# Kernel tuning notes

Measured on AMD Instinct MI355X. Metric: run time of the kernel, lower is better.

The kernel has to match this reference:

```python
import jax, jax.numpy as jnp
import numpy as np

H = 12  # num_heads


def setup_inputs() -> dict:
    key = jax.random.key(0)
    ks = jax.random.split(key, 5)
    B, N, C = 4, 1025, 768
    x = jax.random.normal(ks[0], (B, N, C), jnp.float32)
    g_info = jax.random.normal(ks[1], (2, 2, C), jnp.float32)
    # parameters (torch Linear equivalents, pre-transposed to x @ W layout)
    w_qkv = jax.random.normal(ks[2], (C, 3 * C), jnp.float32) * (C ** -0.5)
    w_proj = jax.random.normal(ks[3], (C, C), jnp.float32) * (C ** -0.5)
    b_proj = jax.random.normal(ks[4], (C,), jnp.float32) * 0.02
    return {"x": x, "g_info": g_info, "w_qkv": w_qkv, "w_proj": w_proj, "b_proj": b_proj}


def _forward(x, g_info, w_qkv, w_proj, b_proj):
    B, N, C = x.shape
    Dh = C // H
    qkv = (x @ w_qkv).reshape(B, N, 3, H, Dh)
    q, k, v = qkv[:, :, 0], qkv[:, :, 1], qkv[:, :, 2]  # (B,N,H,Dh)

    # grounding query from first g_info layer, row 0
    q_g = g_info[0].reshape(-1, H, Dh)[0]  # (H,Dh)

    # num_reserved = 1 (cls token); "pure" = patch tokens
    q_pure = q[:, 1:]  # (B,M,H,Dh)
    qn = q_pure / jnp.linalg.norm(q_pure, axis=-1, keepdims=True)
    qgn = q_g / jnp.linalg.norm(q_g, axis=-1, keepdims=True)
    q_sim = (qn * qgn).sum(-1).mean(-1)  # (B,M): cosine sim averaged over heads
    q_sim = (q_sim - q_sim.min()) / (q_sim.max() - q_sim.min())  # global min-max norm
    pos = q_sim > 0.9   # (B,M) per-batch routing mask
    neg = ~pos
    # a token index is kept in a group if ANY batch element routes it there
    keep_pos = pos.any(axis=0)  # (M,)
    keep_neg = neg.any(axis=0)

    scale = Dh ** -0.5  # xformers memory_efficient_attention internal scale

    def group_attn(gmask, keep):
        # gmask (B,M) bool; keep (M,) bool. Faithful to the torch gather:
        # kept-but-other-batch tokens participate with ZEROED q/k/v.
        m = gmask[..., None, None].astype(x.dtype)  # (B,M,1,1)
        qg = jnp.concatenate([q[:, :1], q_pure * m], axis=1)      # (B,N,H,Dh)
        kg = jnp.concatenate([k[:, :1], k[:, 1:] * m], axis=1)
        vg = jnp.concatenate([v[:, :1], v[:, 1:] * m], axis=1)
        key_keep = jnp.concatenate([jnp.ones((1,), bool), keep])  # cls always kept
        logits = jnp.einsum('bqhd,bkhd->bhqk', qg, kg) * scale
        logits = jnp.where(key_keep[None, None, None, :], logits, -jnp.inf)
        attn = jax.nn.softmax(logits, axis=-1)
        return jnp.einsum('bhqk,bkhd->bqhd', attn, vg)  # (B,N,H,Dh)

    out_pos = group_attn(pos, keep_pos)
    out_neg = group_attn(neg, keep_neg)

    # indices in neither group stay zero (cannot happen since pos|neg covers all).
    body = jnp.where(keep_neg[None, :, None, None], out_neg[:, 1:],
                     jnp.where(keep_pos[None, :, None, None], out_pos[:, 1:],
                               jnp.zeros_like(out_pos[:, 1:])))
    cls = (out_pos[:, :1] + out_neg[:, :1]) * 0.5
    xo = jnp.concatenate([cls, body], axis=1).reshape(B, N, C)
    return xo @ w_proj + b_proj


def reference(x, g_info, w_qkv, w_proj, b_proj):
    return (_forward(x, g_info, w_qkv, w_proj, b_proj), g_info[1:])
```

## Files before the change

kernel.cpp:

```cpp
#include <hip/hip_runtime.h>
#include <math.h>

typedef unsigned short ushort_t;
typedef short s16x8 __attribute__((ext_vector_type(8)));
typedef float f32x4 __attribute__((ext_vector_type(4)));

#define MFMA16(a, b, c) __builtin_amdgcn_mfma_f32_16x16x32_bf16(a, b, c, 0, 0, 0)

#define BATCH 4
#define SEQ   1025
#define CH    768
#define HEADS 12
#define NBH   48
#define NKPAD 1088
#define NTILE 17
#define NQB   34
#define MROWS 4100
#define SCALE2 0.18033688011112042f

__device__ __forceinline__ ushort_t f2bf(float f) {
    unsigned u = __builtin_bit_cast(unsigned, f);
    u += 0x7FFFu + ((u >> 16) & 1u);
    return (ushort_t)(u >> 16);
}
__device__ __forceinline__ unsigned cvt_pk_bf16(float lo, float hi) {
    unsigned r;
    asm("v_cvt_pk_bf16_f32 %0, %1, %2" : "=v"(r) : "v"(lo), "v"(hi));
    return r;
}
__device__ __forceinline__ float max3f(float a, float b, float c) {
    float r;
    asm("v_max3_f32 %0, %1, %2, %3" : "=v"(r) : "v"(a), "v"(b), "v"(c));
    return r;
}
__device__ __forceinline__ float fast_exp2(float x) {
    float r; asm("v_exp_f32 %0, %1" : "=v"(r) : "v"(x)); return r;
}

__global__ __launch_bounds__(256) void gemm_f32(
    const float* __restrict__ A, const float* __restrict__ Bm,
    float* __restrict__ Cm, int M, int K, int ldb, int Nn)
{
    __shared__ float As[32][68];
    __shared__ float Bs[32][64];
    int t = threadIdx.x;
    int m0 = blockIdx.y * 64, n0 = blockIdx.x * 64;
    int ty = t >> 4, tx = t & 15;
    int laRow = t >> 2, laK = (t & 3) * 4;
    int lbK = t >> 4, lbN = (t & 15) * 4;
    float acc[4][4] = {};
    for (int k0 = 0; k0 < K; k0 += 32) {
        int arow = m0 + laRow;
        #pragma unroll
        for (int half = 0; half < 2; ++half) {
            float4 av = make_float4(0.f, 0.f, 0.f, 0.f);
            if (arow < M) av = *(const float4*)(A + (size_t)arow * K + k0 + laK + 16 * half);
            As[laK + 16 * half + 0][laRow] = av.x;
            As[laK + 16 * half + 1][laRow] = av.y;
            As[laK + 16 * half + 2][laRow] = av.z;
            As[laK + 16 * half + 3][laRow] = av.w;
            *(float4*)&Bs[lbK + 16 * half][lbN] =
                *(const float4*)(Bm + (size_t)(k0 + lbK + 16 * half) * ldb + n0 + lbN);
        }
        __syncthreads();
        #pragma unroll
        for (int kk = 0; kk < 32; ++kk) {
            float4 a4 = *(const float4*)&As[kk][ty * 4];
            float4 b4 = *(const float4*)&Bs[kk][tx * 4];
            float a[4] = {a4.x, a4.y, a4.z, a4.w};
            float b[4] = {b4.x, b4.y, b4.z, b4.w};
            #pragma unroll
            for (int i = 0; i < 4; ++i)
                #pragma unroll
                for (int j = 0; j < 4; ++j) acc[i][j] += a[i] * b[j];
        }
        __syncthreads();
    }
    #pragma unroll
    for (int i = 0; i < 4; ++i) {
        int row = m0 + ty * 4 + i;
        if (row >= M) continue;
        #pragma unroll
        for (int j = 0; j < 4; ++j)
            Cm[(size_t)row * Nn + n0 + tx * 4 + j] = acc[i][j];
    }
}

__global__ __launch_bounds__(256) void convx(const float* __restrict__ x,
                                             ushort_t* __restrict__ xb, int n4)
{
    int i = blockIdx.x * 256 + threadIdx.x;
    if (i >= n4) return;
    float4 v = ((const float4*)x)[i];
    ushort_t o[4] = {f2bf(v.x), f2bf(v.y), f2bf(v.z), f2bf(v.w)};
    *(uint2*)(xb + (size_t)i * 4) = *(const uint2*)o;
}

__global__ __launch_bounds__(256) void convT(const float* __restrict__ src, int ld,
                                             int c0, ushort_t* __restrict__ dst)
{
    __shared__ float tile[32][33];
    int k0 = blockIdx.x * 32, n0 = blockIdx.y * 32;
    int t = threadIdx.x, tx = t & 31, ty = t >> 5;
    #pragma unroll
    for (int i = 0; i < 32; i += 8)
        tile[ty + i][tx] = src[(size_t)(k0 + ty + i) * ld + c0 + n0 + tx];
    __syncthreads();
    #pragma unroll
    for (int i = 0; i < 32; i += 8)
        dst[(size_t)(n0 + ty + i) * CH + k0 + tx] = f2bf(tile[tx][ty + i]);
}

__global__ __launch_bounds__(256) void qconv(const float* __restrict__ qf,
                                             ushort_t* __restrict__ qtb)
{
    int i = blockIdx.x * 256 + threadIdx.x;
    if (i >= MROWS * CH / 8) return;
    int row = i / (CH / 8);
    int rem = i % (CH / 8);
    int b = row / SEQ, tok = row % SEQ;
    int h = rem >> 3, d8 = (rem & 7) * 8;
    const float* src = qf + (size_t)row * CH + h * 64 + d8;
    ushort_t o[8];
    #pragma unroll
    for (int j = 0; j < 8; ++j) o[j] = f2bf(src[j]);
    *(uint4*)(qtb + ((size_t)(b * HEADS + h) * NKPAD + tok) * 64 + d8) =
        *(const uint4*)o;
}

template<int MODE>
__global__ __launch_bounds__(256) void mfma_gemm(
    const ushort_t* __restrict__ A, const ushort_t* __restrict__ B,
    ushort_t* __restrict__ kbuf, ushort_t* __restrict__ vtbuf,
    const float* __restrict__ bias, float* __restrict__ outp)
{
    __shared__ __align__(16) ushort_t As[128][40];
    __shared__ __align__(16) ushort_t Bs[64][40];
    const int NT = (MODE == 0) ? 24 : 12;
    int t = threadIdx.x, w = t >> 6, l = t & 63;
    int l15 = l & 15, lhi = l >> 4;
    int wr = w >> 1, wc = w & 1;

    int lin = blockIdx.x, logical;
    if (MODE == 0) {
        logical = (lin & 7) * 99 + (lin >> 3);
    } else {
        int xcd = lin & 7, idx = lin >> 3;
        logical = (xcd < 4 ? xcd * 50 : 200 + (xcd - 4) * 49) + idx;
    }
    int m0 = (logical / NT) * 128;
    int n0 = (logical % NT) * 64;

    int trow = t >> 2, tcol = (t & 3) * 8;
    f32x4 acc[4][2] = {};

    for (int k0 = 0; k0 < CH; k0 += 32) {
        uint4 a0v = make_uint4(0, 0, 0, 0), a1v = make_uint4(0, 0, 0, 0);
        int ar0 = m0 + trow, ar1 = m0 + trow + 64;
        if (ar0 < MROWS) a0v = *(const uint4*)(A + (size_t)ar0 * CH + k0 + tcol);
        if (ar1 < MROWS) a1v = *(const uint4*)(A + (size_t)ar1 * CH + k0 + tcol);
        uint4 bv = *(const uint4*)(B + (size_t)(n0 + trow) * CH + k0 + tcol);
        if (k0) __syncthreads();
        *(uint4*)&As[trow][tcol] = a0v;
        *(uint4*)&As[trow + 64][tcol] = a1v;
        *(uint4*)&Bs[trow][tcol] = bv;
        __syncthreads();
        s16x8 af[4], bf[2];
        #pragma unroll
        for (int i = 0; i < 4; ++i)
            af[i] = *(const s16x8*)&As[wr * 64 + 16 * i + l15][lhi * 8];
        #pragma unroll
        for (int j = 0; j < 2; ++j)
            bf[j] = *(const s16x8*)&Bs[wc * 32 + 16 * j + l15][lhi * 8];
        #pragma unroll
        for (int i = 0; i < 4; ++i)
            #pragma unroll
            for (int j = 0; j < 2; ++j)
                acc[i][j] = MFMA16(af[i], bf[j], acc[i][j]);
    }

    #pragma unroll
    for (int i = 0; i < 4; ++i)
        #pragma unroll
        for (int j = 0; j < 2; ++j)
            #pragma unroll
            for (int r = 0; r < 4; ++r) {
                int m = m0 + wr * 64 + 16 * i + lhi * 4 + r;
                if (m >= MROWS) continue;
                int n = n0 + wc * 32 + 16 * j + l15;
                if (MODE == 0) {
                    ushort_t val = f2bf(acc[i][j][r]);
                    int b_ = m / SEQ, tok = m % SEQ;
                    if (n < CH) {
                        int h = n >> 6, d = n & 63;
                        kbuf[((size_t)(b_ * HEADS + h) * NKPAD + tok) * 64 + d] = val;
                    } else {
                        int c = n - CH, h = c >> 6, d = c & 63;
                        vtbuf[((size_t)(b_ * HEADS + h) * 64 + d) * NKPAD + tok] = val;
                    }
                } else {
                    outp[(size_t)m * CH + n] = acc[i][j][r] + bias[n];
                }
            }
}

__global__ __launch_bounds__(256) void zeropad(ushort_t* kbuf, ushort_t* vtbuf, ushort_t* qtb)
{
    int t = blockIdx.x * 256 + threadIdx.x;
    if (t < NBH * 63 * 64) {
        int bh = t / (63 * 64), rem = t % (63 * 64);
        kbuf[((size_t)bh * NKPAD + 1025 + rem / 64) * 64 + (rem & 63)] = 0;
        qtb [((size_t)bh * NKPAD + 1025 + rem / 64) * 64 + (rem & 63)] = 0;
    }
    if (t < NBH * 64 * 63) {
        int bh = t / (64 * 63), rem = t % (64 * 63);
        vtbuf[((size_t)bh * 64 + rem / 63) * NKPAD + 1025 + rem % 63] = 0;
    }
}

__global__ __launch_bounds__(64) void qsim_kernel(
    const float* __restrict__ qf, const float* __restrict__ g, float* __restrict__ qsim)
{
    int idx = blockIdx.x;
    int b = idx >> 10, j = idx & 1023, n = j + 1;
    int lane = threadIdx.x;
    const float* qrow = qf + (size_t)(b * SEQ + n) * CH;
    float acc = 0.f;
    for (int h = 0; h < HEADS; ++h) {
        float qv = qrow[h * 64 + lane];
        float gv = g[h * 64 + lane];
        float sqg = qv * gv, sqq = qv * qv, sgg = gv * gv;
        #pragma unroll
        for (int off = 32; off; off >>= 1) {
            sqg += __shfl_xor(sqg, off);
            sqq += __shfl_xor(sqq, off);
            sgg += __shfl_xor(sgg, off);
        }
        acc += sqg / sqrtf(sqq * sgg);
    }
    if (lane == 0) qsim[idx] = acc * (1.0f / HEADS);
}

__global__ __launch_bounds__(1024) void mask_kernel(
    const float* __restrict__ qsim, unsigned char* __restrict__ posm,
    unsigned char* __restrict__ vgrp,
    unsigned long long* __restrict__ actbits, float* __restrict__ n0arr)
{
    __shared__ float wmin[16], wmax[16];
    __shared__ unsigned int sbm[4 * 2 * 34];
    __shared__ int scnt[8];
    int t = threadIdx.x;
    if (t < 4 * 2 * 34) sbm[t] = 0u;
    if (t < 8) scnt[t] = 0;
    float v[4];
    float lmin = 1e30f, lmax = -1e30f;
    #pragma unroll
    for (int b = 0; b < 4; ++b) {
        v[b] = qsim[b * 1024 + t];
        lmin = fminf(lmin, v[b]); lmax = fmaxf(lmax, v[b]);
    }
    #pragma unroll
    for (int off = 32; off; off >>= 1) {
        lmin = fminf(lmin, __shfl_xor(lmin, off));
        lmax = fmaxf(lmax, __shfl_xor(lmax, off));
    }
    if ((t & 63) == 0) { wmin[t >> 6] = lmin; wmax[t >> 6] = lmax; }
    __syncthreads();
    if (t == 0) {
        float gmin = wmin[0], gmax = wmax[0];
        for (int i = 1; i < 16; ++i) { gmin = fminf(gmin, wmin[i]); gmax = fmaxf(gmax, wmax[i]); }
        wmin[0] = gmin; wmax[0] = gmax;
    }
    __syncthreads();
    float gmin = wmin[0], den = wmax[0] - gmin;
    int pb[4], anyp = 0, anyn = 0;
    #pragma unroll
    for (int b = 0; b < 4; ++b) {
        float s = (v[b] - gmin) / den;
        pb[b] = s > 0.9f ? 1 : 0;
        anyp |= pb[b]; anyn |= (1 - pb[b]);
    }
    int k = t + 1;
    int wd = k >> 5;
    unsigned bit = 1u << (k & 31);
    #pragma unroll
    for (int b = 0; b < 4; ++b) {
        if (pb[b]) atomicOr(&sbm[(b * 2 + 0) * 34 + wd], bit);
        else       atomicOr(&sbm[(b * 2 + 1) * 34 + wd], bit);
        unsigned long long bp = __ballot(anyp && !pb[b]);
        unsigned long long bn = __ballot(anyn && pb[b]);
        if ((t & 63) == 0) {
            atomicAdd(&scnt[b * 2 + 0], (int)__popcll(bp));
            atomicAdd(&scnt[b * 2 + 1], (int)__popcll(bn));
        }
        posm[b * 1024 + t] = (unsigned char)pb[b];
    }
    vgrp[2 + t] = (unsigned char)anyn;
    if (t < 2) vgrp[t] = (unsigned char)t;
    if (t < 62) vgrp[1026 + t] = 0;
    __syncthreads();
    if (t < 4 * 2 * 34) {
        unsigned vv = sbm[t];
        if ((t % 34) == 0) vv |= 1u;
        ((unsigned int*)actbits)[t] = vv;
    }
    if (t < 8) n0arr[t] = (float)scnt[t];
}

__global__ __launch_bounds__(256) void attn_mfma(
    const ushort_t* __restrict__ qtb, const ushort_t* __restrict__ kb,
    const ushort_t* __restrict__ vtb,
    const unsigned long long* __restrict__ actbits,
    const float* __restrict__ n0arr,
    const unsigned char* __restrict__ vgrp,
    const unsigned char* __restrict__ posm,
    ushort_t* __restrict__ xob, float* __restrict__ clsf)
{
    __shared__ __align__(16) float comb[4][64][18];

    int t = threadIdx.x, w = t >> 6, l = t & 63;
    int l15 = l & 15, lhi = l >> 4;

    int lin = blockIdx.y * NQB + blockIdx.x;
    int xcd = lin & 7, slot = lin >> 3;
    int bh = xcd * 6 + slot / NQB;
    int qb = slot % NQB;
    int b = bh / HEADS, h = bh % HEADS;

    int qv0 = qb * 32 + l15;
    int qv1 = qv0 + 16;
    int g0 = vgrp[qv0], g1 = vgrp[qv1];
    float n00 = n0arr[b * 2 + g0], n01 = n0arr[b * 2 + g1];
    float mq0 = 1.f, mq1 = 1.f;
    if (qv0 >= 2) {
        int j = qv0 - 2; if (j > 1023) j = 1023;
        int p = posm[b * 1024 + j];
        mq0 = (float)(g0 ? 1 - p : p);
    }
    {
        int j = qv1 - 2; if (j > 1023) j = 1023;
        int p = posm[b * 1024 + j];
        mq1 = (float)(g1 ? 1 - p : p);
    }
    float scl0 = SCALE2 * mq0, scl1 = SCALE2 * mq1;
    const unsigned long long* abp = actbits + (size_t)b * 2 * NTILE;
    const unsigned long long* abn = abp + NTILE;

    int tok0 = (qv0 < 2) ? 0 : qv0 - 1;
    int tok1 = qv1 - 1;
    const ushort_t* qbb = qtb + (size_t)bh * NKPAD * 64 + lhi * 8;
    s16x8 bqA0 = *(const s16x8*)(qbb + (size_t)tok0 * 64);
    s16x8 bqA1 = *(const s16x8*)(qbb + (size_t)tok0 * 64 + 32);
    s16x8 bqB0 = *(const s16x8*)(qbb + (size_t)tok1 * 64);
    s16x8 bqB1 = *(const s16x8*)(qbb + (size_t)tok1 * 64 + 32);

    f32x4 out0[4] = {{0,0,0,0},{0,0,0,0},{0,0,0,0},{0,0,0,0}};
    f32x4 out1[4] = {{0,0,0,0},{0,0,0,0},{0,0,0,0},{0,0,0,0}};
    float mrow0 = -INFINITY, lrow0 = 0.f;
    float mrow1 = -INFINITY, lrow1 = 0.f;

    const ushort_t* kp = kb + (size_t)bh * NKPAD * 64 + (size_t)w * 4096 + l15 * 64 + lhi * 8;
    const ushort_t* vp = vtb + (size_t)bh * 64 * NKPAD + (size_t)l15 * NKPAD + w * 64 + lhi * 8;
    ushort_t* pw = (ushort_t*)&comb[0][0][0] + w * 2048;
    int swz = (l15 & 7) << 3;

    for (int tile = w; tile < NTILE; tile += 4) {
        s16x8 kf[8], vf[8];
        #pragma unroll
        for (int tt = 0; tt < 4; ++tt) {
            kf[2 * tt]     = *(const s16x8*)(kp + 1024 * tt);
            kf[2 * tt + 1] = *(const s16x8*)(kp + 1024 * tt + 32);
        }
        #pragma unroll
        for (int dt = 0; dt < 4; ++dt) {
            const ushort_t* vpd = vp + (size_t)(16 * NKPAD) * dt;
            vf[2 * dt]     = *(const s16x8*)vpd;
            vf[2 * dt + 1] = *(const s16x8*)(vpd + 32);
        }
        f32x4 s0[4], s1[4];
        #pragma unroll
        for (int tt = 0; tt < 4; ++tt) {
            f32x4 a0 = {0, 0, 0, 0}, a1 = {0, 0, 0, 0};
            a0 = MFMA16(kf[2 * tt], bqA0, a0);
            a0 = MFMA16(kf[2 * tt + 1], bqA1, a0);
            a1 = MFMA16(kf[2 * tt], bqB0, a1);
            a1 = MFMA16(kf[2 * tt + 1], bqB1, a1);
            s0[tt] = a0; s1[tt] = a1;
        }
        unsigned long long amp_ = abp[tile], amn_ = abn[tile];
        {
            unsigned long long am = g0 ? amn_ : amp_;
            #pragma unroll
            for (int tt = 0; tt < 4; ++tt) {
                unsigned nib = (unsigned)(am >> (16 * tt + 4 * lhi)) & 0xFu;
                #pragma unroll
                for (int r = 0; r < 4; ++r)
                    s0[tt][r] = ((nib >> r) & 1u) ? s0[tt][r] * scl0 : -INFINITY;
            }
            float ma = max3f(s0[0][0], s0[0][1], s0[0][2]);
            float mb = max3f(s0[0][3], s0[1][0], s0[1][1]);
            float mc = max3f(s0[1][2], s0[1][3], s0[2][0]);
            float md = max3f(s0[2][1], s0[2][2], s0[2][3]);
            float me = max3f(s0[3][0], s0[3][1], s0[3][2]);
            float smax = fmaxf(max3f(ma, mb, mc), max3f(md, me, s0[3][3]));
            smax = fmaxf(smax, __shfl_xor(smax, 16));
            smax = fmaxf(smax, __shfl_xor(smax, 32));
            float mnew = fmaxf(mrow0, smax);
            float msafe = (mnew == -INFINITY) ? 0.f : mnew;
            float alpha = fast_exp2(mrow0 - msafe);
            mrow0 = mnew;
            #pragma unroll
            for (int tt = 0; tt < 4; ++tt)
                #pragma unroll
                for (int r = 0; r < 4; ++r)
                    s0[tt][r] = fast_exp2(s0[tt][r] - msafe);
            float l0 = (s0[0][0] + s0[0][1]) + (s0[0][2] + s0[0][3]);
            float l1 = (s0[1][0] + s0[1][1]) + (s0[1][2] + s0[1][3]);
            float l2 = (s0[2][0] + s0[2][1]) + (s0[2][2] + s0[2][3]);
            float l3 = (s0[3][0] + s0[3][1]) + (s0[3][2] + s0[3][3]);
            float ls = (l0 + l1) + (l2 + l3);
            ls += __shfl_xor(ls, 16);
            ls += __shfl_xor(ls, 32);
            lrow0 = lrow0 * alpha + ls;
            #pragma unroll
            for (int dt = 0; dt < 4; ++dt) out0[dt] *= alpha;
            #pragma unroll
            for (int tt = 0; tt < 4; ++tt) {
                unsigned lo = cvt_pk_bf16(s0[tt][0], s0[tt][1]);
                unsigned hi = cvt_pk_bf16(s0[tt][2], s0[tt][3]);
                int kk = 16 * tt + 4 * lhi;
                *(uint2*)&pw[(l15 * 64 + kk) ^ swz] = make_uint2(lo, hi);
            }
        }
        {
            unsigned long long am = g1 ? amn_ : amp_;
            #pragma unroll
            for (int tt = 0; tt < 4; ++tt) {
                unsigned nib = (unsigned)(am >> (16 * tt + 4 * lhi)) & 0xFu;
                #pragma unroll
                for (int r = 0; r < 4; ++r)
                    s1[tt][r] = ((nib >> r) & 1u) ? s1[tt][r] * scl1 : -INFINITY;
            }
            float ma = max3f(s1[0][0], s1[0][1], s1[0][2]);
            float mb = max3f(s1[0][3], s1[1][0], s1[1][1]);
            float mc = max3f(s1[1][2], s1[1][3], s1[2][0]);
            float md = max3f(s1[2][1], s1[2][2], s1[2][3]);
            float me = max3f(s1[3][0], s1[3][1], s1[3][2]);
            float smax = fmaxf(max3f(ma, mb, mc), max3f(md, me, s1[3][3]));
            smax = fmaxf(smax, __shfl_xor(smax, 16));
            smax = fmaxf(smax, __shfl_xor(smax, 32));
            float mnew = fmaxf(mrow1, smax);
            float msafe = (mnew == -INFINITY) ? 0.f : mnew;
            float alpha = fast_exp2(mrow1 - msafe);
            mrow1 = mnew;
            #pragma unroll
            for (int tt = 0; tt < 4; ++tt)
                #pragma unroll
                for (int r = 0; r < 4; ++r)
                    s1[tt][r] = fast_exp2(s1[tt][r] - msafe);
            float l0 = (s1[0][0] + s1[0][1]) + (s1[0][2] + s1[0][3]);
            float l1 = (s1[1][0] + s1[1][1]) + (s1[1][2] + s1[1][3]);
            float l2 = (s1[2][0] + s1[2][1]) + (s1[2][2] + s1[2][3]);
            float l3 = (s1[3][0] + s1[3][1]) + (s1[3][2] + s1[3][3]);
            float ls = (l0 + l1) + (l2 + l3);
            ls += __shfl_xor(ls, 16);
            ls += __shfl_xor(ls, 32);
            lrow1 = lrow1 * alpha + ls;
            #pragma unroll
            for (int dt = 0; dt < 4; ++dt) out1[dt] *= alpha;
            #pragma unroll
            for (int tt = 0; tt < 4; ++tt) {
                unsigned lo = cvt_pk_bf16(s1[tt][0], s1[tt][1]);
                unsigned hi = cvt_pk_bf16(s1[tt][2], s1[tt][3]);
                int kk = 16 * tt + 4 * lhi;
                *(uint2*)&pw[1024 + ((l15 * 64 + kk) ^ swz)] = make_uint2(lo, hi);
            }
        }
        s16x8 pa0 = *(const s16x8*)&pw[(l15 * 64 + lhi * 8) ^ swz];
        s16x8 pa1 = *(const s16x8*)&pw[(l15 * 64 + 32 + lhi * 8) ^ swz];
        s16x8 pb0 = *(const s16x8*)&pw[1024 + ((l15 * 64 + lhi * 8) ^ swz)];
        s16x8 pb1 = *(const s16x8*)&pw[1024 + ((l15 * 64 + 32 + lhi * 8) ^ swz)];
        #pragma unroll
        for (int dt = 0; dt < 4; ++dt) {
            out0[dt] = MFMA16(vf[2 * dt], pa0, out0[dt]);
            out0[dt] = MFMA16(vf[2 * dt + 1], pa1, out0[dt]);
            out1[dt] = MFMA16(vf[2 * dt], pb0, out1[dt]);
            out1[dt] = MFMA16(vf[2 * dt + 1], pb1, out1[dt]);
        }
        kp += 4 * 4096;
        vp += 4 * 64;
    }

    #pragma unroll
    for (int pass = 0; pass < 2; ++pass) {
        __syncthreads();
        {
            const f32x4* o = pass ? out1 : out0;
            #pragma unroll
            for (int dt = 0; dt < 4; ++dt) *(f32x4*)&comb[w][l][4 * dt] = o[dt];
            comb[w][l][16] = pass ? mrow1 : mrow0;
            comb[w][l][17] = pass ? lrow1 : lrow0;
        }
        __syncthreads();
        if (w == 0) {
            int qv = pass ? qv1 : qv0;
            float n0 = pass ? n01 : n00;
            float M = fmaxf(fmaxf(comb[0][l][16], comb[1][l][16]),
                            fmaxf(comb[2][l][16], comb[3][l][16]));
            if (n0 > 0.f) M = fmaxf(M, 0.f);
            float L = n0 * fast_exp2(0.f - M);
            f32x4 o[4] = {{0,0,0,0},{0,0,0,0},{0,0,0,0},{0,0,0,0}};
            #pragma unroll
            for (int w2 = 0; w2 < 4; ++w2) {
                float a = fast_exp2(comb[w2][l][16] - M);
                L += comb[w2][l][17] * a;
                #pragma unroll
                for (int dt = 0; dt < 4; ++dt)
                    o[dt] += *(const f32x4*)&comb[w2][l][4 * dt] * a;
            }
            float invl = 1.0f / L;
            if (qv <= 1025) {
                if (qv >= 2) {
                    int n = qv - 1;
                    ushort_t* dst = xob + (size_t)(b * SEQ + n) * CH + h * 64 + 4 * lhi;
                    #pragma unroll
                    for (int dt = 0; dt < 4; ++dt) {
                        unsigned lo = cvt_pk_bf16(o[dt][0] * invl, o[dt][1] * invl);
                        unsigned hi = cvt_pk_bf16(o[dt][2] * invl, o[dt][3] * invl);
                        *(uint2*)(dst + 16 * dt) = make_uint2(lo, hi);
                    }
                } else {
                    float* dst = clsf + (size_t)(qv * BATCH + b) * CH + h * 64 + 4 * lhi;
                    #pragma unroll
                    for (int dt = 0; dt < 4; ++dt)
                        #pragma unroll
                        for (int r = 0; r < 4; ++r)
                            dst[16 * dt + r] = o[dt][r] * invl;
                }
            }
        }
    }
}

__global__ __launch_bounds__(768) void cls_combine(
    const float* __restrict__ clsf, ushort_t* __restrict__ xob)
{
    int b = blockIdx.x, c = threadIdx.x;
    float v = 0.5f * (clsf[(size_t)b * CH + c] + clsf[(size_t)(BATCH + b) * CH + c]);
    xob[(size_t)b * SEQ * CH + c] = f2bf(v);
}

extern "C" void kernel_launch(void* const* d_in, const int* in_sizes, int n_in,
                              void* d_out, int out_size, void* d_ws, size_t ws_size,
                              hipStream_t stream) {
    const float* x      = (const float*)d_in[0];
    const float* g_info = (const float*)d_in[1];
    const float* w_qkv  = (const float*)d_in[2];
    const float* w_proj = (const float*)d_in[3];
    const float* b_proj = (const float*)d_in[4];
    float* out = (float*)d_out;
    char* ws = (char*)d_ws;

    size_t off = 0;
    auto alloc = [&](size_t bytes) { size_t o = off; off += (bytes + 255) & ~(size_t)255; return o; };
    float*    qf    = (float*)(ws + alloc((size_t)MROWS * CH * 4));
    ushort_t* xb    = (ushort_t*)(ws + alloc((size_t)MROWS * CH * 2));
    ushort_t* wkvT  = (ushort_t*)(ws + alloc((size_t)2 * CH * CH * 2));
    ushort_t* wpT   = (ushort_t*)(ws + alloc((size_t)CH * CH * 2));
    ushort_t* qtb   = (ushort_t*)(ws + alloc((size_t)NBH * NKPAD * 64 * 2));
    ushort_t* kbuf  = (ushort_t*)(ws + alloc((size_t)NBH * NKPAD * 64 * 2));
    ushort_t* vtbuf = (ushort_t*)(ws + alloc((size_t)NBH * NKPAD * 64 * 2));
    ushort_t* xob   = (ushort_t*)(ws + alloc((size_t)MROWS * CH * 2));
    float*    clsf  = (float*)(ws + alloc((size_t)2 * BATCH * CH * 4));
    float*    qsim  = (float*)(ws + alloc((size_t)BATCH * 1024 * 4));
    unsigned char* posm = (unsigned char*)(ws + alloc((size_t)BATCH * 1024));
    unsigned long long* actbits = (unsigned long long*)(ws + alloc((size_t)BATCH * 2 * NTILE * 8));
    float* n0arr = (float*)(ws + alloc((size_t)8 * 4));
    unsigned char* vgrp = (unsigned char*)(ws + alloc((size_t)NKPAD));

    convx<<<(MROWS * CH / 4 + 255) / 256, 256, 0, stream>>>(x, xb, MROWS * CH / 4);
    convT<<<dim3(CH / 32, 2 * CH / 32), 256, 0, stream>>>(w_qkv, 3 * CH, CH, wkvT);
    convT<<<dim3(CH / 32, CH / 32), 256, 0, stream>>>(w_proj, CH, 0, wpT);
    zeropad<<<(NBH * 64 * 63 + 255) / 256, 256, 0, stream>>>(kbuf, vtbuf, qtb);

    gemm_f32<<<dim3(CH / 64, (MROWS + 63) / 64), 256, 0, stream>>>(
        x, w_qkv, qf, MROWS, CH, 3 * CH, CH);
    mfma_gemm<0><<<792, 256, 0, stream>>>(xb, wkvT, kbuf, vtbuf, nullptr, nullptr);

    qsim_kernel<<<BATCH * 1024, 64, 0, stream>>>(qf, g_info, qsim);
    mask_kernel<<<1, 1024, 0, stream>>>(qsim, posm, vgrp, actbits, n0arr);
    qconv<<<(MROWS * CH / 8 + 255) / 256, 256, 0, stream>>>(qf, qtb);

    attn_mfma<<<dim3(NQB, NBH), 256, 0, stream>>>(
        qtb, kbuf, vtbuf, actbits, n0arr, vgrp, posm, xob, clsf);
    cls_combine<<<BATCH, CH, 0, stream>>>(clsf, xob);

    mfma_gemm<1><<<396, 256, 0, stream>>>(xob, wpT, nullptr, nullptr, b_proj, out);

    hipMemcpyAsync(out + (size_t)MROWS * CH, g_info + 2 * CH, (size_t)2 * CH * sizeof(float),
                   hipMemcpyDeviceToDevice, stream);
}
```

Baseline: 245.7 us.

## Double-buffer fp32 Q GEMM tiles and remap blocks for XCD locality

The fp32 Q-projection GEMM now keeps two shared-memory tile buffers. The next K-slice is prefetched into registers while the current slice is computed, and one barrier per iteration replaces the previous two. The launch also becomes a 1D grid whose block ids are remapped so that each XCD processes a contiguous range of output tiles, which should improve L2 reuse. The cost is doubled LDS use per block and extra registers for the prefetch, which may lower occupancy.

```diff
diff --git a/kernel.cpp b/kernel.cpp
--- a/kernel.cpp
+++ b/kernel.cpp
@@ -41,32 +41,55 @@
     const float* __restrict__ A, const float* __restrict__ Bm,
     float* __restrict__ Cm, int M, int K, int ldb, int Nn)
 {
-    __shared__ float As[32][68];
-    __shared__ float Bs[32][64];
+    __shared__ float As[2][32][68];
+    __shared__ float Bs[2][32][64];
     int t = threadIdx.x;
-    int m0 = blockIdx.y * 64, n0 = blockIdx.x * 64;
+
+    int lin = blockIdx.x;
+    int xcd = lin & 7, idx = lin >> 3;
+    int logical = (xcd < 4 ? xcd * 98 : 392 + (xcd - 4) * 97) + idx;
+    int m0 = (logical / 12) * 64, n0 = (logical % 12) * 64;
+
     int ty = t >> 4, tx = t & 15;
     int laRow = t >> 2, laK = (t & 3) * 4;
     int lbK = t >> 4, lbN = (t & 15) * 4;
     float acc[4][4] = {};
+    float4 avr0, avr1, bvr0, bvr1;
+
+    int arow = m0 + laRow;
+    avr0 = make_float4(0.f, 0.f, 0.f, 0.f);
+    avr1 = avr0;
+    if (arow < M) {
+        avr0 = *(const float4*)(A + (size_t)arow * K + laK);
+        avr1 = *(const float4*)(A + (size_t)arow * K + laK + 16);
+    }
+    bvr0 = *(const float4*)(Bm + (size_t)(lbK) * ldb + n0 + lbN);
+    bvr1 = *(const float4*)(Bm + (size_t)(lbK + 16) * ldb + n0 + lbN);
+    As[0][laK + 0][laRow] = avr0.x; As[0][laK + 1][laRow] = avr0.y;
+    As[0][laK + 2][laRow] = avr0.z; As[0][laK + 3][laRow] = avr0.w;
+    As[0][laK + 16][laRow] = avr1.x; As[0][laK + 17][laRow] = avr1.y;
+    As[0][laK + 18][laRow] = avr1.z; As[0][laK + 19][laRow] = avr1.w;
+    *(float4*)&Bs[0][lbK][lbN] = bvr0;
+    *(float4*)&Bs[0][lbK + 16][lbN] = bvr1;
+    __syncthreads();
+
     for (int k0 = 0; k0 < K; k0 += 32) {
-        int arow = m0 + laRow;
-        #pragma unroll
-        for (int half = 0; half < 2; ++half) {
-            float4 av = make_float4(0.f, 0.f, 0.f, 0.f);
-            if (arow < M) av = *(const float4*)(A + (size_t)arow * K + k0 + laK + 16 * half);
-            As[laK + 16 * half + 0][laRow] = av.x;
-            As[laK + 16 * half + 1][laRow] = av.y;
-            As[laK + 16 * half + 2][laRow] = av.z;
-            As[laK + 16 * half + 3][laRow] = av.w;
-            *(float4*)&Bs[lbK + 16 * half][lbN] =
-                *(const float4*)(Bm + (size_t)(k0 + lbK + 16 * half) * ldb + n0 + lbN);
-        }
-        __syncthreads();
+        int cur = (k0 >> 5) & 1;
+        int kn = k0 + 32;
+        if (kn < K) {
+            avr0 = make_float4(0.f, 0.f, 0.f, 0.f);
+            avr1 = avr0;
+            if (arow < M) {
+                avr0 = *(const float4*)(A + (size_t)arow * K + kn + laK);
+                avr1 = *(const float4*)(A + (size_t)arow * K + kn + laK + 16);
+            }
+            bvr0 = *(const float4*)(Bm + (size_t)(kn + lbK) * ldb + n0 + lbN);
+            bvr1 = *(const float4*)(Bm + (size_t)(kn + lbK + 16) * ldb + n0 + lbN);
+        }
         #pragma unroll
         for (int kk = 0; kk < 32; ++kk) {
-            float4 a4 = *(const float4*)&As[kk][ty * 4];
-            float4 b4 = *(const float4*)&Bs[kk][tx * 4];
+            float4 a4 = *(const float4*)&As[cur][kk][ty * 4];
+            float4 b4 = *(const float4*)&Bs[cur][kk][tx * 4];
             float a[4] = {a4.x, a4.y, a4.z, a4.w};
             float b[4] = {b4.x, b4.y, b4.z, b4.w};
             #pragma unroll
@@ -74,7 +97,16 @@
                 #pragma unroll
                 for (int j = 0; j < 4; ++j) acc[i][j] += a[i] * b[j];
         }
-        __syncthreads();
+        if (kn < K) {
+            int nxt = cur ^ 1;
+            As[nxt][laK + 0][laRow] = avr0.x; As[nxt][laK + 1][laRow] = avr0.y;
+            As[nxt][laK + 2][laRow] = avr0.z; As[nxt][laK + 3][laRow] = avr0.w;
+            As[nxt][laK + 16][laRow] = avr1.x; As[nxt][laK + 17][laRow] = avr1.y;
+            As[nxt][laK + 18][laRow] = avr1.z; As[nxt][laK + 19][laRow] = avr1.w;
+            *(float4*)&Bs[nxt][lbK][lbN] = bvr0;
+            *(float4*)&Bs[nxt][lbK + 16][lbN] = bvr1;
+            __syncthreads();
+        }
     }
     #pragma unroll
     for (int i = 0; i < 4; ++i) {
@@ -583,8 +615,7 @@
     convT<<<dim3(CH / 32, CH / 32), 256, 0, stream>>>(w_proj, CH, 0, wpT);
     zeropad<<<(NBH * 64 * 63 + 255) / 256, 256, 0, stream>>>(kbuf, vtbuf, qtb);
 
-    gemm_f32<<<dim3(CH / 64, (MROWS + 63) / 64), 256, 0, stream>>>(
-        x, w_qkv, qf, MROWS, CH, 3 * CH, CH);
+    gemm_f32<<<780, 256, 0, stream>>>(x, w_qkv, qf, MROWS, CH, 3 * CH, CH);
     mfma_gemm<0><<<792, 256, 0, stream>>>(xb, wkvT, kbuf, vtbuf, nullptr, nullptr);
 
     qsim_kernel<<<BATCH * 1024, 64, 0, stream>>>(qf, g_info, qsim);
```

Measured after the change: 246.5 us. No clear change (+0.3%).

## Enlarge fp32 Q-projection GEMM tiles to 128x128 with XCD-aware block mapping

Applied to the files above, without the earlier changes.

The fp32 SIMT GEMM that computes Q now uses 128x128 output tiles with an 8x8 per-thread register accumulator instead of 64x64 with 4x4. This cuts shared-memory traffic per FMA, and it loads global data into registers before the barrier so one barrier per k-step can be dropped. A 1D grid of 198 blocks is remapped so that contiguous logical tiles land on the same XCD, which should improve L2 locality. The trade-offs are higher register pressure and fewer blocks (198), which may underfill the GPU's CUs.

```diff
diff --git a/kernel.cpp b/kernel.cpp
--- a/kernel.cpp
+++ b/kernel.cpp
@@ -41,48 +41,61 @@
     const float* __restrict__ A, const float* __restrict__ Bm,
     float* __restrict__ Cm, int M, int K, int ldb, int Nn)
 {
-    __shared__ float As[32][68];
-    __shared__ float Bs[32][64];
+    __shared__ float As[32][132];
+    __shared__ float Bs[32][132];
     int t = threadIdx.x;
-    int m0 = blockIdx.y * 64, n0 = blockIdx.x * 64;
+
+    int lin = blockIdx.x;
+    int xcd = lin & 7, idx = lin >> 3;
+    int logical = (xcd < 6 ? xcd * 25 : 150 + (xcd - 6) * 24) + idx;
+    int m0 = (logical / 6) * 128, n0 = (logical % 6) * 128;
+
     int ty = t >> 4, tx = t & 15;
-    int laRow = t >> 2, laK = (t & 3) * 4;
-    int lbK = t >> 4, lbN = (t & 15) * 4;
-    float acc[4][4] = {};
+    int laRow = t >> 1, laK = (t & 1) * 16;
+    int lbK = t >> 3, lbC = (t & 7) * 16;
+    float acc[8][8] = {};
+
     for (int k0 = 0; k0 < K; k0 += 32) {
+        float4 av[4], bv[4];
         int arow = m0 + laRow;
         #pragma unroll
-        for (int half = 0; half < 2; ++half) {
-            float4 av = make_float4(0.f, 0.f, 0.f, 0.f);
-            if (arow < M) av = *(const float4*)(A + (size_t)arow * K + k0 + laK + 16 * half);
-            As[laK + 16 * half + 0][laRow] = av.x;
-            As[laK + 16 * half + 1][laRow] = av.y;
-            As[laK + 16 * half + 2][laRow] = av.z;
-            As[laK + 16 * half + 3][laRow] = av.w;
-            *(float4*)&Bs[lbK + 16 * half][lbN] =
-                *(const float4*)(Bm + (size_t)(k0 + lbK + 16 * half) * ldb + n0 + lbN);
+        for (int i = 0; i < 4; ++i) {
+            av[i] = make_float4(0.f, 0.f, 0.f, 0.f);
+            if (arow < M)
+                av[i] = *(const float4*)(A + (size_t)arow * K + k0 + laK + 4 * i);
+            bv[i] = *(const float4*)(Bm + (size_t)(k0 + lbK) * ldb + n0 + lbC + 4 * i);
+        }
+        if (k0) __syncthreads();
+        #pragma unroll
+        for (int i = 0; i < 4; ++i) {
+            As[laK + 4 * i + 0][laRow] = av[i].x;
+            As[laK + 4 * i + 1][laRow] = av[i].y;
+            As[laK + 4 * i + 2][laRow] = av[i].z;
+            As[laK + 4 * i + 3][laRow] = av[i].w;
+            *(float4*)&Bs[lbK][lbC + 4 * i] = bv[i];
         }
         __syncthreads();
         #pragma unroll
         for (int kk = 0; kk < 32; ++kk) {
-            float4 a4 = *(const float4*)&As[kk][ty * 4];
-            float4 b4 = *(const float4*)&Bs[kk][tx * 4];
-            float a[4] = {a4.x, a4.y, a4.z, a4.w};
-            float b[4] = {b4.x, b4.y, b4.z, b4.w};
-            #pragma unroll
-            for (int i = 0; i < 4; ++i)
+            float a[8], b[8];
+            *(float4*)&a[0] = *(const float4*)&As[kk][ty * 8];
+            *(float4*)&a[4] = *(const float4*)&As[kk][ty * 8 + 4];
+            *(float4*)&b[0] = *(const float4*)&Bs[kk][tx * 8];
+            *(float4*)&b[4] = *(const float4*)&Bs[kk][tx * 8 + 4];
+            #pragma unroll
+            for (int i = 0; i < 8; ++i)
                 #pragma unroll
-                for (int j = 0; j < 4; ++j) acc[i][j] += a[i] * b[j];
-        }
-        __syncthreads();
-    }
-    #pragma unroll
-    for (int i = 0; i < 4; ++i) {
-        int row = m0 + ty * 4 + i;
+                for (int j = 0; j < 8; ++j) acc[i][j] += a[i] * b[j];
+        }
+    }
+    #pragma unroll
+    for (int i = 0; i < 8; ++i) {
+        int row = m0 + ty * 8 + i;
         if (row >= M) continue;
-        #pragma unroll
-        for (int j = 0; j < 4; ++j)
-            Cm[(size_t)row * Nn + n0 + tx * 4 + j] = acc[i][j];
+        *(float4*)(Cm + (size_t)row * Nn + n0 + tx * 8) =
+            make_float4(acc[i][0], acc[i][1], acc[i][2], acc[i][3]);
+        *(float4*)(Cm + (size_t)row * Nn + n0 + tx * 8 + 4) =
+            make_float4(acc[i][4], acc[i][5], acc[i][6], acc[i][7]);
     }
 }
 
@@ -583,8 +596,7 @@
     convT<<<dim3(CH / 32, CH / 32), 256, 0, stream>>>(w_proj, CH, 0, wpT);
     zeropad<<<(NBH * 64 * 63 + 255) / 256, 256, 0, stream>>>(kbuf, vtbuf, qtb);
 
-    gemm_f32<<<dim3(CH / 64, (MROWS + 63) / 64), 256, 0, stream>>>(
-        x, w_qkv, qf, MROWS, CH, 3 * CH, CH);
+    gemm_f32<<<198, 256, 0, stream>>>(x, w_qkv, qf, MROWS, CH, 3 * CH, CH);
     mfma_gemm<0><<<792, 256, 0, stream>>>(xb, wkvT, kbuf, vtbuf, nullptr, nullptr);
 
     qsim_kernel<<<BATCH * 1024, 64, 0, stream>>>(qf, g_info, qsim);
```

Measured after the change: 281.7 us. 1.15x slower.
